# Kernel optimization log

Measured on AMD Instinct MI355X. Metric: run time of the kernel, lower is better.

## Reference

```python
import jax, jax.numpy as jnp
import numpy as np

B, H, L, D = 2, 16, 2048, 64


def setup_inputs() -> dict:
    key = jax.random.key(0)
    kq, kk, kv = jax.random.split(key, 3)
    q = jax.random.normal(kq, (B, H, L, D), dtype=jnp.float32)
    k = jax.random.normal(kk, (B, H, L, D), dtype=jnp.float32)
    v = jax.random.normal(kv, (B, H, L, D), dtype=jnp.float32)
    return {"q": q, "k": k, "v": v}


def reference(q, k, v):
    use_norm = True
    seq_len = q.shape[-2]
    scale = q.shape[-1] ** (-0.5)
    q = q * scale
    # [B, H, L, L] score matrix
    attn = jnp.einsum("bhqd,bhkd->bhqk", q, k)
    # 2nd-order Taylor expansion of exp: 1 + s + 0.5*s^2
    attn = 1.0 + attn + 0.5 * attn * attn
    # causal mask (lower-triangular kept)
    causal = jnp.tril(jnp.ones((seq_len, seq_len), dtype=bool))
    attn = jnp.where(causal, attn, 0.0)
    o = jnp.einsum("bhqk,bhkd->bhqd", attn, v)
    if use_norm:
        z = attn.sum(-1)
        o = o / (z[..., None] + 1e-06)
    return o
```

## Files before the change

### kernel.cpp

```cpp
#include <hip/hip_runtime.h>
#include <hip/hip_bf16.h>

typedef __bf16    bf16x8  __attribute__((ext_vector_type(8)));
typedef __bf16    bf16x4  __attribute__((ext_vector_type(4)));
typedef _Float16  half8   __attribute__((ext_vector_type(8)));
typedef _Float16  half4   __attribute__((ext_vector_type(4)));
typedef _Float16  half2   __attribute__((ext_vector_type(2)));
typedef float     floatx4 __attribute__((ext_vector_type(4)));

constexpr int Bc  = 2;
constexpr int Hc  = 16;
constexpr int Lc  = 2048;
constexpr int Dc  = 64;
constexpr int BHn = Bc * Hc;
constexpr int BM  = 128;
constexpr int BN  = 128;
constexpr int NQT = Lc / BM;
constexpr int LDK = 72;
constexpr int LDV = 136;
constexpr int SMEM_BYTES = 35840;

static __device__ __forceinline__ half2 pack_f16(float a, float b) {
    return __builtin_bit_cast(half2, __builtin_amdgcn_cvt_pkrtz(a, b));
}

__global__ void prep(const float* __restrict__ kp, const float* __restrict__ vp,
                     __bf16* __restrict__ k16, _Float16* __restrict__ v16) {
    const int bid = blockIdx.x, tid = threadIdx.x;
    if (bid < 1024) {
        const size_t base = (size_t)bid * 4096 + tid * 4;
        #pragma unroll
        for (int rep = 0; rep < 4; ++rep) {
            const size_t i = base + rep * 1024;
            floatx4 v = *(const floatx4*)(kp + i);
            bf16x4 b;
            b[0] = (__bf16)v[0]; b[1] = (__bf16)v[1]; b[2] = (__bf16)v[2]; b[3] = (__bf16)v[3];
            *(bf16x4*)(k16 + i) = b;
        }
    } else {
        const int vb  = bid - 1024;
        const int bh  = vb >> 5, kt = vb & 31;
        const int key = kt * 64 + (tid & 63);
        const int k5  = key & 31;
        const int pcol = (key & ~31) | (((k5 >> 2) & 3) * 8 + ((k5 >> 4) & 1) * 4 + (k5 & 3));
        const int d0  = (tid >> 6) * 16;
        const float* src = vp + ((size_t)bh * Lc + key) * Dc;
        _Float16*    dst = v16 + (size_t)bh * Dc * Lc + pcol;
        #pragma unroll
        for (int i = 0; i < 16; ++i) {
            const int d = d0 + i;
            dst[(size_t)d * Lc] = (_Float16)src[d];
        }
    }
}

__global__ __launch_bounds__(256, 2)
void taylor_attn(const float* __restrict__ qp, const __bf16* __restrict__ k16,
                 const _Float16* __restrict__ v16, float* __restrict__ op)
{
    __shared__ __align__(16) char smem[SMEM_BYTES];
    __bf16*   Ks = (__bf16*)smem;
    _Float16* VT = (_Float16*)(smem + 18432);

    const int tid  = threadIdx.x;
    const int wv   = tid >> 6;
    const int lane = tid & 63;
    const int lm   = lane & 15;
    const int quad = lane >> 4;
    const int wq   = wv >> 1;
    const int wk   = wv & 1;

    const int cu    = (int)(blockIdx.x & 255);
    const int snd   = (int)(blockIdx.x >> 8);
    const int bh    = cu & 31;
    const int qslot = cu >> 5;
    const int qi    = snd ? qslot : (NQT - 1 - qslot);
    const int q0    = qi * BM;
    const int jmax  = qi;

    const float*    qbase = qp  + ((size_t)bh * Lc + q0) * Dc;
    const __bf16*   kj    = k16 + (size_t)bh * Lc * Dc;
    const _Float16* vj    = v16 + (size_t)bh * Dc * Lc;

    bf16x8 kr[4]; half8 vr[4];
    #pragma unroll
    for (int rep = 0; rep < 4; ++rep)
        kr[rep] = *(const bf16x8*)(kj + 8 * (tid + 256 * rep));
    #pragma unroll
    for (int rep = 0; rep < 4; ++rep) {
        const int g = tid + 256 * rep;
        vr[rep] = *(const half8*)(vj + (size_t)(g >> 4) * Lc + (g & 15) * 8);
    }

    {
        const int r0 = tid >> 4, c4 = tid & 15;
        #pragma unroll
        for (int rep = 0; rep < 8; ++rep) {
            const int row = r0 + rep * 16;
            floatx4 v = *(const floatx4*)(qbase + row * Dc + c4 * 4);
            bf16x4 b;
            b[0] = (__bf16)v[0]; b[1] = (__bf16)v[1]; b[2] = (__bf16)v[2]; b[3] = (__bf16)v[3];
            *(bf16x4*)&Ks[row * LDK + c4 * 4] = b;
        }
    }
    __syncthreads();
    bf16x8 qa[4][2];
    #pragma unroll
    for (int st = 0; st < 4; ++st)
        #pragma unroll
        for (int kf = 0; kf < 2; ++kf)
            qa[st][kf] = *(const bf16x8*)&Ks[(64 * wq + 16 * st + lm) * LDK + kf * 32 + quad * 8];
    __syncthreads();

    floatx4 oacc[4][4] = {};
    floatx4 zacc[4]    = {};

    const half8 ones = {(_Float16)1.f, (_Float16)1.f, (_Float16)1.f, (_Float16)1.f,
                        (_Float16)1.f, (_Float16)1.f, (_Float16)1.f, (_Float16)1.f};
    const half2 c8  = {(_Float16)0.125f, (_Float16)0.125f};
    const half2 c1  = {(_Float16)1.f,    (_Float16)1.f};
    const half2 ch  = {(_Float16)0.5f,   (_Float16)0.5f};

    for (int j = 0; j <= jmax; ++j) {
        #pragma unroll
        for (int rep = 0; rep < 4; ++rep) {
            const int c = tid + 256 * rep;
            *(bf16x8*)&Ks[(c >> 3) * LDK + (c & 7) * 8] = kr[rep];
        }
        #pragma unroll
        for (int rep = 0; rep < 4; ++rep) {
            const int g = tid + 256 * rep;
            *(half8*)&VT[(g >> 4) * LDV + (g & 15) * 8] = vr[rep];
        }
        __syncthreads();

        if (j < jmax) {
            kj += BN * Dc;
            vj += BN;
            #pragma unroll
            for (int rep = 0; rep < 4; ++rep)
                kr[rep] = *(const bf16x8*)(kj + 8 * (tid + 256 * rep));
            #pragma unroll
            for (int rep = 0; rep < 4; ++rep) {
                const int g = tid + 256 * rep;
                vr[rep] = *(const half8*)(vj + (size_t)(g >> 4) * Lc + (g & 15) * 8);
            }
        }

        const bool nm = (j == jmax);
        #pragma unroll
        for (int hf = 0; hf < 2; ++hf) {
            const int grp = 2 * wk + hf;

            floatx4 sacc[4][2] = {};
            #pragma unroll
            for (int kb4 = 0; kb4 < 2; ++kb4) {
                const int row0 = 16 * (4 * wk + 2 * hf + kb4);
                #pragma unroll
                for (int kf = 0; kf < 2; ++kf) {
                    bf16x8 ka = *(const bf16x8*)&Ks[(row0 + lm) * LDK + kf * 32 + quad * 8];
                    #pragma unroll
                    for (int st = 0; st < 4; ++st)
                        sacc[st][kb4] = __builtin_amdgcn_mfma_f32_16x16x32_bf16(ka, qa[st][kf], sacc[st][kb4], 0, 0, 0);
                }
            }

            half8 wf[4];
            #pragma unroll
            for (int st = 0; st < 4; ++st) {
                const int thr = q0 + 64 * wq + 16 * st + lm - j * BN;
                half2 wh[2][2];
                #pragma unroll
                for (int kb4 = 0; kb4 < 2; ++kb4) {
                    half2 s01 = pack_f16(sacc[st][kb4][0], sacc[st][kb4][1]);
                    half2 s23 = pack_f16(sacc[st][kb4][2], sacc[st][kb4][3]);
                    half2 a01 = s01 * c8 + c1;
                    half2 a23 = s23 * c8 + c1;
                    half2 w01 = a01 * (a01 * ch) + ch;
                    half2 w23 = a23 * (a23 * ch) + ch;
                    if (nm) {
                        const int i0 = 16 * (4 * wk + 2 * hf + kb4) + 4 * quad;
                        w01[0] = (i0 + 0 <= thr) ? w01[0] : (_Float16)0.f;
                        w01[1] = (i0 + 1 <= thr) ? w01[1] : (_Float16)0.f;
                        w23[0] = (i0 + 2 <= thr) ? w23[0] : (_Float16)0.f;
                        w23[1] = (i0 + 3 <= thr) ? w23[1] : (_Float16)0.f;
                    }
                    wh[kb4][0] = w01;
                    wh[kb4][1] = w23;
                }
                half4 lo = __builtin_shufflevector(wh[0][0], wh[0][1], 0, 1, 2, 3);
                half4 hi = __builtin_shufflevector(wh[1][0], wh[1][1], 0, 1, 2, 3);
                wf[st] = __builtin_shufflevector(lo, hi, 0, 1, 2, 3, 4, 5, 6, 7);
            }

            #pragma unroll
            for (int db = 0; db < 4; ++db) {
                half8 va = *(const half8*)&VT[(16 * db + lm) * LDV + 32 * grp + 8 * quad];
                #pragma unroll
                for (int st = 0; st < 4; ++st)
                    oacc[st][db] = __builtin_amdgcn_mfma_f32_16x16x32_f16(va, wf[st], oacc[st][db], 0, 0, 0);
            }
            #pragma unroll
            for (int st = 0; st < 4; ++st)
                zacc[st] = __builtin_amdgcn_mfma_f32_16x16x32_f16(ones, wf[st], zacc[st], 0, 0, 0);
        }
        __syncthreads();
    }

    float* Ored = (float*)smem;
    float* zred = (float*)(smem + 34816);
    if (wk) {
        #pragma unroll
        for (int st = 0; st < 4; ++st) {
            const int r = wq * 64 + 16 * st + lm;
            #pragma unroll
            for (int db = 0; db < 4; ++db)
                *(floatx4*)&Ored[(size_t)r * 68 + 16 * db + 4 * quad] = oacc[st][db];
            zred[r] = zacc[st][0];
        }
    }
    __syncthreads();
    if (!wk) {
        #pragma unroll
        for (int st = 0; st < 4; ++st) {
            const int r = wq * 64 + 16 * st + lm;
            const float inv = 1.0f / (zacc[st][0] + zred[r] + 1e-6f);
            const int qrow = q0 + 64 * wq + 16 * st + lm;
            float* orow = op + ((size_t)bh * Lc + qrow) * Dc;
            #pragma unroll
            for (int db = 0; db < 4; ++db) {
                floatx4 part = *(const floatx4*)&Ored[(size_t)r * 68 + 16 * db + 4 * quad];
                floatx4 t = (oacc[st][db] + part) * inv;
                *(floatx4*)&orow[16 * db + 4 * quad] = t;
            }
        }
    }
}

extern "C" void kernel_launch(void* const* d_in, const int* in_sizes, int n_in,
                              void* d_out, int out_size, void* d_ws, size_t ws_size,
                              hipStream_t stream) {
    const float* q = (const float*)d_in[0];
    const float* k = (const float*)d_in[1];
    const float* v = (const float*)d_in[2];
    float* o = (float*)d_out;

    __bf16*   k16 = (__bf16*)d_ws;
    _Float16* v16 = (_Float16*)((char*)d_ws + (size_t)BHn * Lc * Dc * 2);

    prep<<<dim3(2048), dim3(256), 0, stream>>>(k, v, k16, v16);
    taylor_attn<<<dim3(NQT * BHn), dim3(256), 0, stream>>>(q, k16, v16, o);
}
```

Measured before the change: 118.3 us.

## Prepack K/V tiles with LDS padding and double-buffer via global_load_lds DMA

```diff
diff --git a/kernel.cpp b/kernel.cpp
--- a/kernel.cpp
+++ b/kernel.cpp
@@ -18,49 +18,66 @@
 constexpr int NQT = Lc / BM;
 constexpr int LDK = 72;
 constexpr int LDV = 136;
-constexpr int SMEM_BYTES = 35840;
+constexpr int KBYTES = BN * LDK * 2;
+constexpr int VBYTES = Dc * LDV * 2;
+constexpr int TILE_BYTES = KBYTES + VBYTES;
+constexpr int TILE_GRANS = TILE_BYTES / 16;
 
 static __device__ __forceinline__ half2 pack_f16(float a, float b) {
     return __builtin_bit_cast(half2, __builtin_amdgcn_cvt_pkrtz(a, b));
 }
 
+static __device__ __forceinline__ void dma16(const void* g, void* l) {
+    __builtin_amdgcn_global_load_lds(
+        (const __attribute__((address_space(1))) void*)g,
+        (__attribute__((address_space(3))) void*)l, 16, 0, 0);
+}
+
 __global__ void prep(const float* __restrict__ kp, const float* __restrict__ vp,
-                     __bf16* __restrict__ k16, _Float16* __restrict__ v16) {
+                     char* __restrict__ kv) {
     const int bid = blockIdx.x, tid = threadIdx.x;
     if (bid < 1024) {
-        const size_t base = (size_t)bid * 4096 + tid * 4;
-        #pragma unroll
-        for (int rep = 0; rep < 4; ++rep) {
-            const size_t i = base + rep * 1024;
-            floatx4 v = *(const floatx4*)(kp + i);
-            bf16x4 b;
-            b[0] = (__bf16)v[0]; b[1] = (__bf16)v[1]; b[2] = (__bf16)v[2]; b[3] = (__bf16)v[3];
-            *(bf16x4*)(k16 + i) = b;
+        const int R    = bid * 64 + (tid >> 2);
+        const int s    = tid & 3;
+        const int bh   = R >> 11;
+        const int key  = R & 2047;
+        const int tile = key >> 7;
+        const int krow = key & 127;
+        const float* src = kp + (size_t)R * 64 + s * 16;
+        char* dst = kv + (size_t)(bh * 16 + tile) * TILE_BYTES + krow * 144 + s * 32;
+        #pragma unroll
+        for (int h = 0; h < 2; ++h) {
+            floatx4 a = *(const floatx4*)(src + h * 8);
+            floatx4 b = *(const floatx4*)(src + h * 8 + 4);
+            bf16x8 o;
+            o[0] = (__bf16)a[0]; o[1] = (__bf16)a[1]; o[2] = (__bf16)a[2]; o[3] = (__bf16)a[3];
+            o[4] = (__bf16)b[0]; o[5] = (__bf16)b[1]; o[6] = (__bf16)b[2]; o[7] = (__bf16)b[3];
+            *(bf16x8*)(dst + h * 16) = o;
         }
     } else {
-        const int vb  = bid - 1024;
-        const int bh  = vb >> 5, kt = vb & 31;
-        const int key = kt * 64 + (tid & 63);
-        const int k5  = key & 31;
-        const int pcol = (key & ~31) | (((k5 >> 2) & 3) * 8 + ((k5 >> 4) & 1) * 4 + (k5 & 3));
-        const int d0  = (tid >> 6) * 16;
+        const int vb   = bid - 1024;
+        const int bh   = vb >> 5, kt = vb & 31;
+        const int key  = kt * 64 + (tid & 63);
+        const int tile = kt >> 1;
+        const int kwt  = (kt & 1) * 64 + (tid & 63);
+        const int k5   = kwt & 31;
+        const int pcol = (kwt & ~31) | (((k5 >> 2) & 3) * 8 + ((k5 >> 4) & 1) * 4 + (k5 & 3));
+        const int d0   = (tid >> 6) * 16;
         const float* src = vp + ((size_t)bh * Lc + key) * Dc;
-        _Float16*    dst = v16 + (size_t)bh * Dc * Lc + pcol;
+        _Float16* dst = (_Float16*)(kv + (size_t)(bh * 16 + tile) * TILE_BYTES + KBYTES);
         #pragma unroll
         for (int i = 0; i < 16; ++i) {
             const int d = d0 + i;
-            dst[(size_t)d * Lc] = (_Float16)src[d];
+            dst[(size_t)d * LDV + pcol] = (_Float16)src[d];
         }
     }
 }
 
 __global__ __launch_bounds__(256, 2)
-void taylor_attn(const float* __restrict__ qp, const __bf16* __restrict__ k16,
-                 const _Float16* __restrict__ v16, float* __restrict__ op)
+void taylor_attn(const float* __restrict__ qp, const char* __restrict__ kv,
+                 float* __restrict__ op)
 {
-    __shared__ __align__(16) char smem[SMEM_BYTES];
-    __bf16*   Ks = (__bf16*)smem;
-    _Float16* VT = (_Float16*)(smem + 18432);
+    __shared__ __align__(16) char smem[2 * TILE_BYTES];
 
     const int tid  = threadIdx.x;
     const int wv   = tid >> 6;
@@ -78,39 +95,49 @@
     const int q0    = qi * BM;
     const int jmax  = qi;
 
-    const float*    qbase = qp  + ((size_t)bh * Lc + q0) * Dc;
-    const __bf16*   kj    = k16 + (size_t)bh * Lc * Dc;
-    const _Float16* vj    = v16 + (size_t)bh * Dc * Lc;
-
-    bf16x8 kr[4]; half8 vr[4];
+    const float* qbase = qp + ((size_t)bh * Lc + q0) * Dc;
+    const char*  kvbh  = kv + (size_t)bh * 16 * TILE_BYTES;
+
+    floatx4 qv[8];
+    const int r0 = tid >> 4, c4 = tid & 15;
     #pragma unroll
-    for (int rep = 0; rep < 4; ++rep)
-        kr[rep] = *(const bf16x8*)(kj + 8 * (tid + 256 * rep));
-    #pragma unroll
-    for (int rep = 0; rep < 4; ++rep) {
-        const int g = tid + 256 * rep;
-        vr[rep] = *(const half8*)(vj + (size_t)(g >> 4) * Lc + (g & 15) * 8);
-    }
+    for (int rep = 0; rep < 8; ++rep)
+        qv[rep] = *(const floatx4*)(qbase + (r0 + rep * 16) * Dc + c4 * 4);
 
     {
-        const int r0 = tid >> 4, c4 = tid & 15;
+        const char* src = kvbh;
+        char* dst = smem;
+        #pragma unroll
+        for (int rep = 0; rep < 8; ++rep)
+            dma16(src + (rep * 256 + tid) * 16, dst + (rep * 256 + tid) * 16);
+        if (tid < 192)
+            dma16(src + (2048 + tid) * 16, dst + (2048 + tid) * 16);
+    }
+
+    {
+        __bf16* Qs = (__bf16*)(smem + TILE_BYTES);
         #pragma unroll
         for (int rep = 0; rep < 8; ++rep) {
-            const int row = r0 + rep * 16;
-            floatx4 v = *(const floatx4*)(qbase + row * Dc + c4 * 4);
             bf16x4 b;
-            b[0] = (__bf16)v[0]; b[1] = (__bf16)v[1]; b[2] = (__bf16)v[2]; b[3] = (__bf16)v[3];
-            *(bf16x4*)&Ks[row * LDK + c4 * 4] = b;
-        }
-    }
-    __syncthreads();
+            b[0] = (__bf16)qv[rep][0]; b[1] = (__bf16)qv[rep][1];
+            b[2] = (__bf16)qv[rep][2]; b[3] = (__bf16)qv[rep][3];
+            *(bf16x4*)&Qs[(r0 + rep * 16) * LDK + c4 * 4] = b;
+        }
+    }
+    asm volatile("s_waitcnt lgkmcnt(0)" ::: "memory");
+    __builtin_amdgcn_s_barrier();
+
     bf16x8 qa[4][2];
-    #pragma unroll
-    for (int st = 0; st < 4; ++st)
-        #pragma unroll
-        for (int kf = 0; kf < 2; ++kf)
-            qa[st][kf] = *(const bf16x8*)&Ks[(64 * wq + 16 * st + lm) * LDK + kf * 32 + quad * 8];
-    __syncthreads();
+    {
+        const __bf16* Qs = (const __bf16*)(smem + TILE_BYTES);
+        #pragma unroll
+        for (int st = 0; st < 4; ++st)
+            #pragma unroll
+            for (int kf = 0; kf < 2; ++kf)
+                qa[st][kf] = *(const bf16x8*)&Qs[(64 * wq + 16 * st + lm) * LDK + kf * 32 + quad * 8];
+    }
+    asm volatile("s_waitcnt lgkmcnt(0)" ::: "memory");
+    __builtin_amdgcn_s_barrier();
 
     floatx4 oacc[4][4] = {};
     floatx4 zacc[4]    = {};
@@ -122,30 +149,24 @@
     const half2 ch  = {(_Float16)0.5f,   (_Float16)0.5f};
 
     for (int j = 0; j <= jmax; ++j) {
-        #pragma unroll
-        for (int rep = 0; rep < 4; ++rep) {
-            const int c = tid + 256 * rep;
-            *(bf16x8*)&Ks[(c >> 3) * LDK + (c & 7) * 8] = kr[rep];
-        }
-        #pragma unroll
-        for (int rep = 0; rep < 4; ++rep) {
-            const int g = tid + 256 * rep;
-            *(half8*)&VT[(g >> 4) * LDV + (g & 15) * 8] = vr[rep];
-        }
-        __syncthreads();
+        const int cur = j & 1;
+        const __bf16*   Kc = (const __bf16*)(smem + cur * TILE_BYTES);
+        const _Float16* Vc = (const _Float16*)(smem + cur * TILE_BYTES + KBYTES);
 
         if (j < jmax) {
-            kj += BN * Dc;
-            vj += BN;
-            #pragma unroll
-            for (int rep = 0; rep < 4; ++rep)
-                kr[rep] = *(const bf16x8*)(kj + 8 * (tid + 256 * rep));
-            #pragma unroll
-            for (int rep = 0; rep < 4; ++rep) {
-                const int g = tid + 256 * rep;
-                vr[rep] = *(const half8*)(vj + (size_t)(g >> 4) * Lc + (g & 15) * 8);
-            }
-        }
+            const char* src = kvbh + (size_t)(j + 1) * TILE_BYTES;
+            char* dst = smem + (cur ^ 1) * TILE_BYTES;
+            #pragma unroll
+            for (int rep = 0; rep < 8; ++rep)
+                dma16(src + (rep * 256 + tid) * 16, dst + (rep * 256 + tid) * 16);
+            if (tid < 192)
+                dma16(src + (2048 + tid) * 16, dst + (2048 + tid) * 16);
+            if (wv < 3) asm volatile("s_waitcnt vmcnt(9)" ::: "memory");
+            else        asm volatile("s_waitcnt vmcnt(8)" ::: "memory");
+        } else {
+            asm volatile("s_waitcnt vmcnt(0)" ::: "memory");
+        }
+        __builtin_amdgcn_s_barrier();
 
         const bool nm = (j == jmax);
         #pragma unroll
@@ -158,7 +179,7 @@
                 const int row0 = 16 * (4 * wk + 2 * hf + kb4);
                 #pragma unroll
                 for (int kf = 0; kf < 2; ++kf) {
-                    bf16x8 ka = *(const bf16x8*)&Ks[(row0 + lm) * LDK + kf * 32 + quad * 8];
+                    bf16x8 ka = *(const bf16x8*)&Kc[(row0 + lm) * LDK + kf * 32 + quad * 8];
                     #pragma unroll
                     for (int st = 0; st < 4; ++st)
                         sacc[st][kb4] = __builtin_amdgcn_mfma_f32_16x16x32_bf16(ka, qa[st][kf], sacc[st][kb4], 0, 0, 0);
@@ -195,7 +216,7 @@
 
             #pragma unroll
             for (int db = 0; db < 4; ++db) {
-                half8 va = *(const half8*)&VT[(16 * db + lm) * LDV + 32 * grp + 8 * quad];
+                half8 va = *(const half8*)&Vc[(16 * db + lm) * LDV + 32 * grp + 8 * quad];
                 #pragma unroll
                 for (int st = 0; st < 4; ++st)
                     oacc[st][db] = __builtin_amdgcn_mfma_f32_16x16x32_f16(va, wf[st], oacc[st][db], 0, 0, 0);
@@ -204,7 +225,9 @@
             for (int st = 0; st < 4; ++st)
                 zacc[st] = __builtin_amdgcn_mfma_f32_16x16x32_f16(ones, wf[st], zacc[st], 0, 0, 0);
         }
-        __syncthreads();
+
+        asm volatile("s_waitcnt lgkmcnt(0)" ::: "memory");
+        __builtin_amdgcn_s_barrier();
     }
 
     float* Ored = (float*)smem;
@@ -245,9 +268,8 @@
     const float* v = (const float*)d_in[2];
     float* o = (float*)d_out;
 
-    __bf16*   k16 = (__bf16*)d_ws;
-    _Float16* v16 = (_Float16*)((char*)d_ws + (size_t)BHn * Lc * Dc * 2);
-
-    prep<<<dim3(2048), dim3(256), 0, stream>>>(k, v, k16, v16);
-    taylor_attn<<<dim3(NQT * BHn), dim3(256), 0, stream>>>(q, k16, v16, o);
-}
+    char* kv = (char*)d_ws;
+
+    prep<<<dim3(2048), dim3(256), 0, stream>>>(k, v, kv);
+    taylor_attn<<<dim3(NQT * BHn), dim3(256), 0, stream>>>(q, kv, o);
+}
```

Result: no change. 117.6 us (-0.6%).
